# Optimization experiments

Hardware: AMD Instinct MI355X
Metric: run time of the kernel (lower is better)

## Reference

```python
import jax, jax.numpy as jnp
import numpy as np

N = 10000        # nodes
E = 320000       # edges (avg degree 32)
IN = 739         # in_channels
C = 64           # hid_channels
H = 1            # heads
D = C // H       # per-head dim
L = 10           # layer_num
G = 64           # num graphs in batch
LAMBD = 1.0


def setup_inputs() -> dict:
    key = jax.random.key(0)
    ks = jax.random.split(key, 14)
    s = 0.05
    return {
        "x": jax.random.normal(ks[0], (N, IN), jnp.float32),
        "edge_index": jax.random.randint(ks[1], (2, E), 0, N, dtype=jnp.int32),
        "batch": jnp.sort(jax.random.randint(ks[2], (N,), 0, G, dtype=jnp.int32)),
        # InitFeat: Linear(739->64), ELU, Linear(64->64) (dropout = identity at eval)
        "w0": jax.random.normal(ks[3], (IN, C), jnp.float32) * s,
        "b0": jax.random.normal(ks[4], (C,), jnp.float32) * s,
        "w1": jax.random.normal(ks[5], (C, C), jnp.float32) * s,
        "b1": jax.random.normal(ks[6], (C,), jnp.float32) * s,
        # AeroConv attention vectors for k = 1..L-1
        "conv_att": jax.random.normal(ks[7], (L - 1, H, D), jnp.float32) * s,
        # UpdateZ k=0 (g = h, width D) and k=1..L-1 (g = [h, z_scale], width 2D)
        "hop_att0": jax.random.normal(ks[8], (H, D), jnp.float32) * s,
        "hop_bias0": jax.random.normal(ks[9], (H,), jnp.float32) * s,
        "hop_att": jax.random.normal(ks[10], (L - 1, H, 2 * D), jnp.float32) * s,
        "hop_bias": jax.random.normal(ks[11], (L - 1, H), jnp.float32) * s,
        # readout head Linear(64->1)
        "w_head": jax.random.normal(ks[12], (C, 1), jnp.float32) * s,
        "b_head": jax.random.normal(ks[13], (1,), jnp.float32) * s,
    }


def reference(x, edge_index, batch, w0, b0, w1, b1, conv_att,
              hop_att0, hop_bias0, hop_att, hop_bias, w_head, b_head):
    src, dst = edge_index[0], edge_index[1]

    # ---- InitFeat (dropout is identity at inference) ----
    h = x @ w0 + b0
    h = jax.nn.elu(h) @ w1 + b1              # [N, C]
    x = h

    # ---- UpdateZ, k = 0: z = h * hop_attention ----
    hh = x.reshape(N, H, D)
    attn = jnp.sum(hop_att0 * jax.nn.elu(hh), axis=-1) + hop_bias0   # [N, H]
    z = hh * attn[..., None]                 # [N, H, D]

    for i in range(L - 1):
        k = i + 1
        scale = jnp.float32(np.log(LAMBD / k + 1.0 + 1e-6))
        z_scale = z * scale                  # [N, H, D]

        # per-edge attention: elu(z_i + z_j), dot with att, softplus
        a = jax.nn.elu(z_scale[src] + z_scale[dst])                   # [E, H, D]
        a = jax.nn.softplus(jnp.sum(conv_att[i] * a, axis=-1)) + 1e-6  # [E, H]

        # symmetric normalization by scatter-summed degree
        adj_sum = jax.ops.segment_sum(a, dst, num_segments=N)         # [N, H]
        inv = jnp.maximum(adj_sum, 1e-32) ** -0.5
        na = (inv[src] * a * inv[dst])[..., None]                     # [E, H, 1]

        # weighted scatter-sum of source features
        msgs = x[src].reshape(E, H, D) * na                           # [E, H, D]
        x = jax.ops.segment_sum(msgs, dst, num_segments=N).reshape(N, C)

        # UpdateZ (k >= 1): g = [h, z_scale]
        hh = x.reshape(N, H, D)
        g = jnp.concatenate([hh, z_scale], axis=-1)                   # [N, H, 2D]
        attn = jnp.sum(hop_att[i] * jax.nn.elu(g), axis=-1) + hop_bias[i]
        z = z + hh * attn[..., None]

    # ---- readout: elu, global mean pool over batch, linear head ----
    zf = jax.nn.elu(z.reshape(N, C))
    seg_sum = jax.ops.segment_sum(zf, batch, num_segments=G)          # [G, C]
    cnt = jax.ops.segment_sum(jnp.ones((N,), zf.dtype), batch, num_segments=G)
    pooled = seg_sum / jnp.maximum(cnt, 1.0)[:, None]
    return pooled @ w_head + b_head                                   # [G, 1]
```

## Files before the change

kernel.cpp:

```cpp
#include <hip/hip_runtime.h>
#include <hip/hip_bf16.h>
#include <math.h>

#define NN     10000
#define EE     320000
#define IN_CH  739
#define CC     64
#define GG     64
#define NLAYER 9
#define NBUCK  157
#define CHUNK  2048

__device__ __forceinline__ float eluf(float x) {
    return x > 0.f ? x : __expf(x) - 1.f;
}
__device__ __forceinline__ float softplusf(float x) {
    return fmaxf(x, 0.f) + __logf(1.f + __expf(-fabsf(x)));
}
__device__ __forceinline__ float wave_sum(float v) {
#pragma unroll
    for (int off = 32; off > 0; off >>= 1) v += __shfl_xor(v, off, 64);
    return v;
}

__global__ __launch_bounds__(256) void k_gemm1_part(
    const float* __restrict__ x, const float* __restrict__ w0,
    float* __restrict__ hpart)
{
    __shared__ float xs[64 * 68];
    __shared__ float ws[64 * 64];
    const int tid = threadIdx.x;
    const int cg = tid & 15;
    const int rg = tid >> 4;
    const int split = blockIdx.x & 3;
    const int R0 = (blockIdx.x >> 2) * 64;
    const int K0 = split * 192;

    const int sk = tid & 63;
    const int sr = tid >> 6;

    float xr[16], wr[16];
    float acc[4][4] = {};

#pragma unroll
    for (int i = 0; i < 16; ++i) {
        const int r = sr + 4 * i;
        const int gr = R0 + r;
        const int gk = K0 + sk;
        xr[i] = (gr < NN && gk < IN_CH) ? x[(size_t)gr * IN_CH + gk] : 0.f;
        const int wk = K0 + r;
        wr[i] = (wk < IN_CH) ? w0[wk * CC + sk] : 0.f;
    }

    for (int t = 0; t < 3; ++t) {
        __syncthreads();
#pragma unroll
        for (int i = 0; i < 16; ++i) {
            const int r = sr + 4 * i;
            xs[r * 68 + sk] = xr[i];
            ws[r * 64 + sk] = wr[i];
        }
        __syncthreads();
        if (t + 1 < 3) {
            const int k0 = K0 + (t + 1) * 64;
#pragma unroll
            for (int i = 0; i < 16; ++i) {
                const int r = sr + 4 * i;
                const int gr = R0 + r;
                const int gk = k0 + sk;
                xr[i] = (gr < NN && gk < IN_CH) ? x[(size_t)gr * IN_CH + gk] : 0.f;
                const int wk = k0 + r;
                wr[i] = (wk < IN_CH) ? w0[wk * CC + sk] : 0.f;
            }
        }
#pragma unroll 4
        for (int k4 = 0; k4 < 64; k4 += 4) {
            float4 xv[4], wv[4];
#pragma unroll
            for (int j = 0; j < 4; ++j)
                xv[j] = *(const float4*)&xs[(rg * 4 + j) * 68 + k4];
#pragma unroll
            for (int q = 0; q < 4; ++q)
                wv[q] = *(const float4*)&ws[(k4 + q) * 64 + cg * 4];
#pragma unroll
            for (int j = 0; j < 4; ++j) {
                const float* xf = (const float*)&xv[j];
#pragma unroll
                for (int q = 0; q < 4; ++q) {
                    const float* wf = (const float*)&wv[q];
#pragma unroll
                    for (int i = 0; i < 4; ++i)
                        acc[j][i] = fmaf(xf[q], wf[i], acc[j][i]);
                }
            }
        }
    }

#pragma unroll
    for (int j = 0; j < 4; ++j) {
        const int row = R0 + rg * 4 + j;
        if (row < NN)
            *(float4*)&hpart[((size_t)split * NN + row) * CC + cg * 4] =
                make_float4(acc[j][0], acc[j][1], acc[j][2], acc[j][3]);
    }
}

__global__ __launch_bounds__(256) void k_init2(
    const float* __restrict__ hpart,
    const float* __restrict__ b0, const float* __restrict__ w1,
    const float* __restrict__ b1,
    const float* __restrict__ hop_att0, const float* __restrict__ hop_bias0,
    float scale1,
    float* __restrict__ xout, float* __restrict__ zout,
    float* __restrict__ zsout)
{
    __shared__ float xs[32 * 68];
    __shared__ float ws[64 * 64];
    const int tid = threadIdx.x;
    const int R0 = blockIdx.x * 32;

#pragma unroll
    for (int j = 0; j < 2; ++j) {
        const int slot = tid + 256 * j;
        const int row = slot >> 4;
        const int col4 = (slot & 15) * 4;
        const int grow = R0 + row;
        float4 s = make_float4(0.f, 0.f, 0.f, 0.f);
        if (grow < NN) {
#pragma unroll
            for (int sp = 0; sp < 4; ++sp) {
                const float4 v =
                    *(const float4*)&hpart[((size_t)sp * NN + grow) * CC + col4];
                s.x += v.x; s.y += v.y; s.z += v.z; s.w += v.w;
            }
        }
        const float4 bb = *(const float4*)&b0[col4];
        s.x = eluf(s.x + bb.x); s.y = eluf(s.y + bb.y);
        s.z = eluf(s.z + bb.z); s.w = eluf(s.w + bb.w);
        *(float4*)&xs[row * 68 + col4] = s;
    }
    {
        const int sk = tid & 63;
        const int sr = tid >> 6;
#pragma unroll
        for (int i = 0; i < 16; ++i)
            ws[(sr + 4 * i) * 64 + sk] = w1[(sr + 4 * i) * CC + sk];
    }
    __syncthreads();

    const int cg = tid & 15;
    const int rg = tid >> 4;
    float acc2[2][4];
    const float4 b1v = *(const float4*)&b1[cg * 4];
#pragma unroll
    for (int j = 0; j < 2; ++j) {
        acc2[j][0] = b1v.x; acc2[j][1] = b1v.y;
        acc2[j][2] = b1v.z; acc2[j][3] = b1v.w;
    }
#pragma unroll 4
    for (int k4 = 0; k4 < 64; k4 += 4) {
        float4 xv[2], wv[4];
#pragma unroll
        for (int j = 0; j < 2; ++j)
            xv[j] = *(const float4*)&xs[(rg * 2 + j) * 68 + k4];
#pragma unroll
        for (int q = 0; q < 4; ++q)
            wv[q] = *(const float4*)&ws[(k4 + q) * 64 + cg * 4];
#pragma unroll
        for (int j = 0; j < 2; ++j) {
            const float* xf = (const float*)&xv[j];
#pragma unroll
            for (int q = 0; q < 4; ++q) {
                const float* wf = (const float*)&wv[q];
#pragma unroll
                for (int i = 0; i < 4; ++i)
                    acc2[j][i] = fmaf(xf[q], wf[i], acc2[j][i]);
            }
        }
    }

    __syncthreads();
#pragma unroll
    for (int j = 0; j < 2; ++j)
        *(float4*)&ws[(rg * 2 + j) * 64 + cg * 4] =
            make_float4(acc2[j][0], acc2[j][1], acc2[j][2], acc2[j][3]);
    __syncthreads();

    const int c = tid & 63;
    const int w = tid >> 6;
    const float ha = hop_att0[c];
    const float hb = hop_bias0[0];
#pragma unroll
    for (int rr = 0; rr < 8; ++rr) {
        const int r = w * 8 + rr;
        const float v = ws[r * 64 + c];
        const float attn = wave_sum(ha * eluf(v)) + hb;
        const int row = R0 + r;
        if (row < NN) {
            const float zv = v * attn;
            xout[row * CC + c] = v;
            zout[row * CC + c] = zv;
            zsout[row * CC + c] = zv * scale1;
        }
    }
}

__global__ __launch_bounds__(256) void k_hist(const int* __restrict__ ei,
                                              int* __restrict__ deg)
{
    const int e = blockIdx.x * 256 + threadIdx.x;
    atomicAdd(&deg[ei[EE + e]], 1);
}

__global__ __launch_bounds__(256) void k_scan(const int* __restrict__ deg,
                                              int* __restrict__ offs,
                                              int* __restrict__ bcur)
{
    __shared__ int part[256];
    const int tid = threadIdx.x;
    const int start = tid * 40;
    const int end = start + 40 < NN ? start + 40 : NN;
    int sum = 0;
    for (int i = start; i < end; ++i) sum += deg[i];
    part[tid] = sum;
    __syncthreads();
    if (tid == 0) {
        int run = 0;
        for (int i = 0; i < 256; ++i) { int t = part[i]; part[i] = run; run += t; }
    }
    __syncthreads();
    int run = part[tid];
    for (int i = start; i < end; ++i) {
        offs[i] = run;
        if ((i & 63) == 0) bcur[i >> 6] = run;
        run += deg[i];
    }
}

__global__ __launch_bounds__(256) void k_part1(
    const int* __restrict__ ei, int* __restrict__ bcur,
    int2* __restrict__ csr_pair)
{
    __shared__ int hist[NBUCK];
    __shared__ int scan_s[NBUCK];
    __shared__ int base_g[NBUCK];
    __shared__ int lcur[NBUCK];
    __shared__ int2 staged[CHUNK];
    const int tid = threadIdx.x;
    const int e0 = blockIdx.x * CHUNK;

    for (int b = tid; b < NBUCK; b += 256) { hist[b] = 0; lcur[b] = 0; }
    __syncthreads();

    int src[8], dst[8];
#pragma unroll
    for (int j = 0; j < 8; ++j) {
        const int e = e0 + tid + 256 * j;
        if (e < EE) {
            src[j] = ei[e];
            dst[j] = ei[EE + e];
            atomicAdd(&hist[dst[j] >> 6], 1);
        } else dst[j] = -1;
    }
    __syncthreads();
    if (tid == 0) {
        int run = 0;
        for (int b = 0; b < NBUCK; ++b) { scan_s[b] = run; run += hist[b]; }
    }
    __syncthreads();
    if (tid < NBUCK && hist[tid] > 0)
        base_g[tid] = atomicAdd(&bcur[tid], hist[tid]);
    __syncthreads();
#pragma unroll
    for (int j = 0; j < 8; ++j) {
        if (dst[j] >= 0) {
            const int b = dst[j] >> 6;
            const int r = atomicAdd(&lcur[b], 1);
            staged[scan_s[b] + r] = make_int2(src[j], dst[j]);
        }
    }
    __syncthreads();
    const int tot = (EE - e0) < CHUNK ? (EE - e0) : CHUNK;
    for (int i = tid; i < tot; i += 256) {
        const int2 p = staged[i];
        const int b = p.y >> 6;
        csr_pair[base_g[b] + (i - scan_s[b])] = p;
    }
}

__global__ __launch_bounds__(256) void k_part2(
    const int* __restrict__ offs, const int2* __restrict__ csr_pair,
    int* __restrict__ csr_src)
{
    __shared__ int lcnt[64];
    __shared__ int loffs[64];
    const int b = blockIdx.x;
    const int tid = threadIdx.x;
    const int d0 = b * 64;
    if (tid < 64) {
        lcnt[tid] = 0;
        const int d = d0 + tid;
        loffs[tid] = (d < NN) ? offs[d] : EE;
    }
    __syncthreads();
    const int r0 = offs[d0];
    const int r1 = (d0 + 64 < NN) ? offs[d0 + 64] : EE;
    for (int i = r0 + tid; i < r1; i += 256) {
        const int2 p = csr_pair[i];
        const int ld = p.y & 63;
        const int r = atomicAdd(&lcnt[ld], 1);
        csr_src[loffs[ld] + r] = p.x;
    }
}

__global__ __launch_bounds__(256) void k_bounds(const int* __restrict__ batch,
                                                int* __restrict__ gstart)
{
    const int n = blockIdx.x * 256 + threadIdx.x;
    if (n >= NN) return;
    if (n == 0)
        for (int g = 0; g <= batch[0]; ++g) gstart[g] = 0;
    else {
        const int b0 = batch[n - 1], b1 = batch[n];
        for (int g = b0 + 1; g <= b1; ++g) gstart[g] = n;
    }
    if (n == NN - 1)
        for (int g = batch[NN - 1] + 1; g <= GG; ++g) gstart[g] = NN;
}

__global__ __launch_bounds__(256) void k_edge_adj(
    const int* __restrict__ offs, const int* __restrict__ deg,
    const int* __restrict__ csr_src,
    const float* __restrict__ zs_buf, const float* __restrict__ conv_att,
    float* __restrict__ a_csr, float* __restrict__ inv_adj)
{
    const int n = blockIdx.x * 4 + (threadIdx.x >> 6);
    const int lane = threadIdx.x & 63;
    const int l = lane & 15;
    const int grp = lane >> 4;
    const int start = offs[n];
    const int len = deg[n];

    const float4 zd = *(const float4*)(zs_buf + n * CC + l * 4);
    const float4 scv = *(const float4*)(conv_att + l * 4);

    float asum = 0.f;
    int i = grp;
    for (; i + 12 < len; i += 16) {
        const int s0 = csr_src[start + i];
        const int s1 = csr_src[start + i + 4];
        const int s2 = csr_src[start + i + 8];
        const int s3 = csr_src[start + i + 12];
        const float4 a0 = *(const float4*)(zs_buf + s0 * CC + l * 4);
        const float4 a1 = *(const float4*)(zs_buf + s1 * CC + l * 4);
        const float4 a2 = *(const float4*)(zs_buf + s2 * CC + l * 4);
        const float4 a3 = *(const float4*)(zs_buf + s3 * CC + l * 4);
        float p0 = scv.x * eluf(a0.x + zd.x);
        p0 = fmaf(scv.y, eluf(a0.y + zd.y), p0);
        p0 = fmaf(scv.z, eluf(a0.z + zd.z), p0);
        p0 = fmaf(scv.w, eluf(a0.w + zd.w), p0);
        float p1 = scv.x * eluf(a1.x + zd.x);
        p1 = fmaf(scv.y, eluf(a1.y + zd.y), p1);
        p1 = fmaf(scv.z, eluf(a1.z + zd.z), p1);
        p1 = fmaf(scv.w, eluf(a1.w + zd.w), p1);
        float p2 = scv.x * eluf(a2.x + zd.x);
        p2 = fmaf(scv.y, eluf(a2.y + zd.y), p2);
        p2 = fmaf(scv.z, eluf(a2.z + zd.z), p2);
        p2 = fmaf(scv.w, eluf(a2.w + zd.w), p2);
        float p3 = scv.x * eluf(a3.x + zd.x);
        p3 = fmaf(scv.y, eluf(a3.y + zd.y), p3);
        p3 = fmaf(scv.z, eluf(a3.z + zd.z), p3);
        p3 = fmaf(scv.w, eluf(a3.w + zd.w), p3);
#pragma unroll
        for (int off = 8; off > 0; off >>= 1) {
            p0 += __shfl_xor(p0, off, 64);
            p1 += __shfl_xor(p1, off, 64);
            p2 += __shfl_xor(p2, off, 64);
            p3 += __shfl_xor(p3, off, 64);
        }
        const float ae0 = softplusf(p0) + 1e-6f;
        const float ae1 = softplusf(p1) + 1e-6f;
        const float ae2 = softplusf(p2) + 1e-6f;
        const float ae3 = softplusf(p3) + 1e-6f;
        asum += ae0 + ae1 + ae2 + ae3;
        if (l == 0) {
            a_csr[start + i] = ae0;
            a_csr[start + i + 4] = ae1;
            a_csr[start + i + 8] = ae2;
            a_csr[start + i + 12] = ae3;
        }
    }
    for (; i < len; i += 4) {
        const int s0 = csr_src[start + i];
        const float4 a0 = *(const float4*)(zs_buf + s0 * CC + l * 4);
        float p0 = scv.x * eluf(a0.x + zd.x);
        p0 = fmaf(scv.y, eluf(a0.y + zd.y), p0);
        p0 = fmaf(scv.z, eluf(a0.z + zd.z), p0);
        p0 = fmaf(scv.w, eluf(a0.w + zd.w), p0);
#pragma unroll
        for (int off = 8; off > 0; off >>= 1) p0 += __shfl_xor(p0, off, 64);
        const float ae0 = softplusf(p0) + 1e-6f;
        asum += ae0;
        if (l == 0) a_csr[start + i] = ae0;
    }

    asum += __shfl_xor(asum, 16, 64);
    asum += __shfl_xor(asum, 32, 64);
    if (lane == 0) inv_adj[n] = rsqrtf(fmaxf(asum, 1e-32f));
}

__global__ __launch_bounds__(256) void k_msg_fused(
    const int* __restrict__ offs, const int* __restrict__ deg,
    const int* __restrict__ csr_src, const float* __restrict__ a_csr,
    const float* __restrict__ inv_adj, const float* __restrict__ x,
    float* __restrict__ xn, float* __restrict__ z,
    float* __restrict__ zs_buf,
    const float* __restrict__ hop_att, const float* __restrict__ hop_bias,
    float scale_next)
{
    const int n = blockIdx.x * 4 + (threadIdx.x >> 6);
    const int c = threadIdx.x & 63;
    const int start = offs[n];
    const int len = deg[n];
    const float invd = inv_adj[n];

    float acc = 0.f;
    for (int base = 0; base < len; base += 64) {
        const int cnt = (len - base) < 64 ? (len - base) : 64;
        int s_l = 0; float na_l = 0.f;
        if (c < cnt) {
            s_l = csr_src[start + base + c];
            na_l = a_csr[start + base + c] * inv_adj[s_l] * invd;
        }
        int j = 0;
        for (; j + 8 <= cnt; j += 8) {
            int ss[8]; float nn_[8];
#pragma unroll
            for (int q = 0; q < 8; ++q) {
                ss[q] = __builtin_amdgcn_readlane(s_l, j + q);
                nn_[q] = __int_as_float(
                    __builtin_amdgcn_readlane(__float_as_int(na_l), j + q));
            }
            float vv[8];
#pragma unroll
            for (int q = 0; q < 8; ++q) vv[q] = x[ss[q] * CC + c];
#pragma unroll
            for (int q = 0; q < 8; ++q) acc = fmaf(vv[q], nn_[q], acc);
        }
        for (; j < cnt; ++j) {
            const int s = __builtin_amdgcn_readlane(s_l, j);
            const float na = __int_as_float(
                __builtin_amdgcn_readlane(__float_as_int(na_l), j));
            acc = fmaf(x[s * CC + c], na, acc);
        }
    }

    const float zv = z[n * CC + c];
    const float zsv = zs_buf[n * CC + c];
    float g = hop_att[c] * eluf(acc) + hop_att[CC + c] * eluf(zsv);
    const float attn = wave_sum(g) + hop_bias[0];
    const float znew = zv + acc * attn;
    z[n * CC + c] = znew;
    zs_buf[n * CC + c] = znew * scale_next;
    xn[n * CC + c] = acc;
}

__global__ __launch_bounds__(256) void k_pool_head(
    const float* __restrict__ z, const int* __restrict__ gstart,
    const float* __restrict__ w_head, const float* __restrict__ b_head,
    float* __restrict__ out)
{
    __shared__ float red[4][CC];
    const int g = blockIdx.x;
    const int w = threadIdx.x >> 6;
    const int c = threadIdx.x & 63;
    const int s0 = gstart[g], s1 = gstart[g + 1];

    float acc = 0.f;
    for (int n = s0 + w; n < s1; n += 4) acc += eluf(z[n * CC + c]);
    red[w][c] = acc;
    __syncthreads();
    if (w == 0) {
        const float v = red[0][c] + red[1][c] + red[2][c] + red[3][c];
        const float tot = wave_sum(v * w_head[c]);
        if (c == 0)
            out[g] = tot / fmaxf((float)(s1 - s0), 1.f) + b_head[0];
    }
}

extern "C" void kernel_launch(void* const* d_in, const int* in_sizes, int n_in,
                              void* d_out, int out_size, void* d_ws, size_t ws_size,
                              hipStream_t stream) {
    const float* x        = (const float*)d_in[0];
    const int*   ei       = (const int*)d_in[1];
    const int*   batch    = (const int*)d_in[2];
    const float* w0       = (const float*)d_in[3];
    const float* b0       = (const float*)d_in[4];
    const float* w1       = (const float*)d_in[5];
    const float* b1       = (const float*)d_in[6];
    const float* conv_att = (const float*)d_in[7];
    const float* hop_att0 = (const float*)d_in[8];
    const float* hop_bias0= (const float*)d_in[9];
    const float* hop_att  = (const float*)d_in[10];
    const float* hop_bias = (const float*)d_in[11];
    const float* w_head   = (const float*)d_in[12];
    const float* b_head   = (const float*)d_in[13];
    float* out = (float*)d_out;

    float sc[NLAYER + 1];
    for (int k = 1; k <= NLAYER; ++k)
        sc[k] = (float)log(1.0 / (double)k + 1.0 + 1e-6);

    float* xA      = (float*)d_ws;
    float* xB      = xA + NN * CC;
    float* zbuf    = xB + NN * CC;
    float* zsbuf   = zbuf + NN * CC;
    float* inv_adj = zsbuf + NN * CC;
    float* hpart   = inv_adj + NN;
    float* a_csr   = hpart;
    int*   csr_src = (int*)(a_csr + EE);
    int2*  csr_pair= (int2*)(csr_src + EE);
    int*   deg     = (int*)(csr_pair + EE);
    int*   offs    = deg + NN;
    int*   bcur    = offs + NN;
    int*   gstart  = bcur + NBUCK;

    k_gemm1_part<<<157 * 4, 256, 0, stream>>>(x, w0, hpart);
    k_init2<<<313, 256, 0, stream>>>(hpart, b0, w1, b1, hop_att0, hop_bias0,
                                     sc[1], xA, zbuf, zsbuf);

    hipMemsetAsync(deg, 0, (size_t)NN * 4, stream);
    k_hist<<<EE / 256, 256, 0, stream>>>(ei, deg);
    k_scan<<<1, 256, 0, stream>>>(deg, offs, bcur);
    k_part1<<<(EE + CHUNK - 1) / CHUNK, 256, 0, stream>>>(ei, bcur, csr_pair);
    k_part2<<<NBUCK, 256, 0, stream>>>(offs, csr_pair, csr_src);
    k_bounds<<<(NN + 255) / 256, 256, 0, stream>>>(batch, gstart);

    float* xcur = xA;
    float* xnext = xB;
    for (int i = 0; i < NLAYER; ++i) {
        const float scale_next = (i + 1 < NLAYER) ? sc[i + 2] : 0.f;
        k_edge_adj<<<NN / 4, 256, 0, stream>>>(offs, deg, csr_src, zsbuf,
                                               conv_att + i * CC,
                                               a_csr, inv_adj);
        k_msg_fused<<<NN / 4, 256, 0, stream>>>(offs, deg, csr_src, a_csr,
                                                inv_adj, xcur, xnext, zbuf,
                                                zsbuf,
                                                hop_att + i * 2 * CC,
                                                hop_bias + i, scale_next);
        float* t = xcur; xcur = xnext; xnext = t;
    }

    k_pool_head<<<GG, 256, 0, stream>>>(zbuf, gstart, w_head, b_head, out);
}
```

Before: 445.1 us.

## Gather messages with float4 loads, four edges per wavefront in parallel

Restructures the per-node message gather so each wavefront splits into four 16-lane groups, each handling a different edge and loading a 256-byte row with float4 loads. Partial sums are combined with cross-group shuffles, and the attention reduction runs over 16 lanes. This replaces the readlane broadcast loop with its scalar per-channel loads and aims for more memory parallelism and fewer instructions. The cost is that every lane now loads its own edge index, and the final stores come only from the first 16 lanes.

```diff
diff --git a/kernel.cpp b/kernel.cpp
--- a/kernel.cpp
+++ b/kernel.cpp
@@ -419,50 +419,75 @@
     float scale_next)
 {
     const int n = blockIdx.x * 4 + (threadIdx.x >> 6);
-    const int c = threadIdx.x & 63;
+    const int lane = threadIdx.x & 63;
+    const int l = lane & 15;
+    const int grp = lane >> 4;
     const int start = offs[n];
     const int len = deg[n];
     const float invd = inv_adj[n];
-
-    float acc = 0.f;
-    for (int base = 0; base < len; base += 64) {
-        const int cnt = (len - base) < 64 ? (len - base) : 64;
-        int s_l = 0; float na_l = 0.f;
-        if (c < cnt) {
-            s_l = csr_src[start + base + c];
-            na_l = a_csr[start + base + c] * inv_adj[s_l] * invd;
-        }
-        int j = 0;
-        for (; j + 8 <= cnt; j += 8) {
-            int ss[8]; float nn_[8];
-#pragma unroll
-            for (int q = 0; q < 8; ++q) {
-                ss[q] = __builtin_amdgcn_readlane(s_l, j + q);
-                nn_[q] = __int_as_float(
-                    __builtin_amdgcn_readlane(__float_as_int(na_l), j + q));
-            }
-            float vv[8];
-#pragma unroll
-            for (int q = 0; q < 8; ++q) vv[q] = x[ss[q] * CC + c];
-#pragma unroll
-            for (int q = 0; q < 8; ++q) acc = fmaf(vv[q], nn_[q], acc);
-        }
-        for (; j < cnt; ++j) {
-            const int s = __builtin_amdgcn_readlane(s_l, j);
-            const float na = __int_as_float(
-                __builtin_amdgcn_readlane(__float_as_int(na_l), j));
-            acc = fmaf(x[s * CC + c], na, acc);
-        }
-    }
-
-    const float zv = z[n * CC + c];
-    const float zsv = zs_buf[n * CC + c];
-    float g = hop_att[c] * eluf(acc) + hop_att[CC + c] * eluf(zsv);
-    const float attn = wave_sum(g) + hop_bias[0];
-    const float znew = zv + acc * attn;
-    z[n * CC + c] = znew;
-    zs_buf[n * CC + c] = znew * scale_next;
-    xn[n * CC + c] = acc;
+    const float4* x4 = (const float4*)x;
+
+    float4 acc = make_float4(0.f, 0.f, 0.f, 0.f);
+    int i = grp;
+    for (; i + 4 < len; i += 8) {
+        const int s0 = csr_src[start + i];
+        const int s1 = csr_src[start + i + 4];
+        const float na0 = a_csr[start + i] * inv_adj[s0] * invd;
+        const float na1 = a_csr[start + i + 4] * inv_adj[s1] * invd;
+        const float4 v0 = x4[s0 * 16 + l];
+        const float4 v1 = x4[s1 * 16 + l];
+        acc.x = fmaf(v0.x, na0, acc.x);
+        acc.y = fmaf(v0.y, na0, acc.y);
+        acc.z = fmaf(v0.z, na0, acc.z);
+        acc.w = fmaf(v0.w, na0, acc.w);
+        acc.x = fmaf(v1.x, na1, acc.x);
+        acc.y = fmaf(v1.y, na1, acc.y);
+        acc.z = fmaf(v1.z, na1, acc.z);
+        acc.w = fmaf(v1.w, na1, acc.w);
+    }
+    for (; i < len; i += 4) {
+        const int s0 = csr_src[start + i];
+        const float na0 = a_csr[start + i] * inv_adj[s0] * invd;
+        const float4 v0 = x4[s0 * 16 + l];
+        acc.x = fmaf(v0.x, na0, acc.x);
+        acc.y = fmaf(v0.y, na0, acc.y);
+        acc.z = fmaf(v0.z, na0, acc.z);
+        acc.w = fmaf(v0.w, na0, acc.w);
+    }
+
+    acc.x += __shfl_xor(acc.x, 16, 64);
+    acc.y += __shfl_xor(acc.y, 16, 64);
+    acc.z += __shfl_xor(acc.z, 16, 64);
+    acc.w += __shfl_xor(acc.w, 16, 64);
+    acc.x += __shfl_xor(acc.x, 32, 64);
+    acc.y += __shfl_xor(acc.y, 32, 64);
+    acc.z += __shfl_xor(acc.z, 32, 64);
+    acc.w += __shfl_xor(acc.w, 32, 64);
+
+    const float4 zv  = *(const float4*)(z + n * CC + l * 4);
+    const float4 zsv = *(const float4*)(zs_buf + n * CC + l * 4);
+    const float4 ha  = *(const float4*)(hop_att + l * 4);
+    const float4 hz  = *(const float4*)(hop_att + CC + l * 4);
+    float gp = ha.x * eluf(acc.x) + ha.y * eluf(acc.y)
+             + ha.z * eluf(acc.z) + ha.w * eluf(acc.w)
+             + hz.x * eluf(zsv.x) + hz.y * eluf(zsv.y)
+             + hz.z * eluf(zsv.z) + hz.w * eluf(zsv.w);
+#pragma unroll
+    for (int off = 8; off > 0; off >>= 1) gp += __shfl_xor(gp, off, 64);
+    const float attn = gp + hop_bias[0];
+
+    if (lane < 16) {
+        float4 znew;
+        znew.x = fmaf(acc.x, attn, zv.x);
+        znew.y = fmaf(acc.y, attn, zv.y);
+        znew.z = fmaf(acc.z, attn, zv.z);
+        znew.w = fmaf(acc.w, attn, zv.w);
+        *(float4*)(z + n * CC + l * 4) = znew;
+        *(float4*)(zs_buf + n * CC + l * 4) =
+            make_float4(znew.x * scale_next, znew.y * scale_next,
+                        znew.z * scale_next, znew.w * scale_next);
+        *(float4*)(xn + n * CC + l * 4) = acc;
+    }
 }
 
 __global__ __launch_bounds__(256) void k_pool_head(
```

Result: no change. 445.4 us (+0.1%).
